# Kernel optimization log

Measured on AMD Instinct MI355X. Metric: run time of the kernel, lower is better.

## Reference

```python
import jax, jax.numpy as jnp
import numpy as np

NUM_HEADS = 16
EMBED_DIM = 1024
HEAD_DIM = EMBED_DIM // NUM_HEADS
DILATION = 4


def setup_inputs() -> dict:
    key = jax.random.key(0)
    ks = jax.random.split(key, 9)
    B, S, E = 2, 4096, EMBED_DIM
    scale = 1.0 / np.sqrt(E)
    inp = {
        "x": jax.random.normal(ks[0], (B, S, E), dtype=jnp.float32),
        "Wq": jax.random.normal(ks[1], (E, E), dtype=jnp.float32) * scale,
        "bq": jnp.zeros((E,), dtype=jnp.float32),
        "Wk": jax.random.normal(ks[2], (E, E), dtype=jnp.float32) * scale,
        "bk": jnp.zeros((E,), dtype=jnp.float32),
        "Wv": jax.random.normal(ks[3], (E, E), dtype=jnp.float32) * scale,
        "bv": jnp.zeros((E,), dtype=jnp.float32),
        "Wo": jax.random.normal(ks[4], (E, E), dtype=jnp.float32) * scale,
        "bo": jnp.zeros((E,), dtype=jnp.float32),
    }
    return inp


def reference(x, Wq, bq, Wk, bk, Wv, bv, Wo, bo):
    B, S, E = x.shape
    H, D = NUM_HEADS, HEAD_DIM

    def split_heads(t):  # [B,S,E] -> [B,H,S,D]
        return t.reshape(B, S, H, D).transpose(0, 2, 1, 3)

    q = split_heads(x @ Wq + bq)
    k = split_heads(x @ Wk + bk)[:, :, ::DILATION, :]   # dilated keys
    v = split_heads(x @ Wv + bv)[:, :, ::DILATION, :]   # dilated values

    scores = jnp.einsum('bhqd,bhkd->bhqk', q, k) / np.sqrt(D).astype(x.dtype)
    attn = jax.nn.softmax(scores, axis=-1)
    ctx = jnp.einsum('bhqk,bhkd->bhqd', attn, v)
    ctx = ctx.transpose(0, 2, 1, 3).reshape(B, S, E)
    return ctx @ Wo + bo
```

## Files before the change

kernel.cpp:

```cpp
#include <hip/hip_runtime.h>
#include <cstdint>
#include <cstddef>

typedef unsigned short u16;
typedef __attribute__((ext_vector_type(4))) float f32x4;
typedef __attribute__((ext_vector_type(8))) short short8;
typedef __attribute__((ext_vector_type(4))) unsigned short u16x4;
typedef short8 __attribute__((may_alias)) short8_a;
typedef uint2 __attribute__((may_alias)) uint2_a;

#define NH 16
#define ED 1024
#define HD 64
#define SEQ 4096
#define SKV 1024

#define QSCALE 0.1803368801111204f

__device__ __forceinline__ u16 f2bf(float f) {
  unsigned u = __builtin_bit_cast(unsigned, f);
  u += 0x7fffu + ((u >> 16) & 1u);
  return (u16)(u >> 16);
}

__device__ __forceinline__ float fexp2(float x) {
  float r;
  asm("v_exp_f32 %0, %1" : "=v"(r) : "v"(x));
  return r;
}

__device__ __forceinline__ unsigned cvtpk(float lo, float hi) {
  unsigned r;
  asm("v_cvt_pk_bf16_f32 %0, %1, %2" : "=v"(r) : "v"(lo), "v"(hi));
  return r;
}

__device__ __forceinline__ void gload16(const void* g, void* l) {
  __builtin_amdgcn_global_load_lds((const __attribute__((address_space(1))) void*)g,
                                   (__attribute__((address_space(3))) void*)l, 16, 0, 0);
}

__device__ __forceinline__ f32x4 mfma16(short8 a, short8 b, f32x4 c) {
  return __builtin_amdgcn_mfma_f32_16x16x32_bf16(a, b, c, 0, 0, 0);
}

__global__ __launch_bounds__(256) void prep_kernel(
    const float* __restrict__ x, u16* __restrict__ x16,
    const float* __restrict__ Wq, const float* __restrict__ Wk,
    const float* __restrict__ Wv, const float* __restrict__ Wo,
    u16* __restrict__ Wqt, u16* __restrict__ Wkt,
    u16* __restrict__ Wvt, u16* __restrict__ Wot) {
  __shared__ float t[64][65];
  int bx = blockIdx.x;
  if (bx < 8192) {
    int i = bx * 256 + threadIdx.x;
    f32x4 v = ((const f32x4*)x)[i];
    u16x4 o;
#pragma unroll
    for (int j = 0; j < 4; ++j) o[j] = f2bf(v[j]);
    ((u16x4*)x16)[i] = o;
    return;
  }
  int tt = bx - 8192;
  int wi = tt >> 8;
  tt &= 255;
  const float* W = (wi == 0) ? Wq : (wi == 1) ? Wk : (wi == 2) ? Wv : Wo;
  u16* Wt = (wi == 0) ? Wqt : (wi == 1) ? Wkt : (wi == 2) ? Wvt : Wot;
  int kb = (tt >> 4) * 64, nb = (tt & 15) * 64;
  int tx = threadIdx.x & 15, ty = threadIdx.x >> 4;
#pragma unroll
  for (int j = 0; j < 4; ++j) {
    int row = ty + j * 16;
    f32x4 v = *(const f32x4*)&W[(size_t)(kb + row) * ED + nb + tx * 4];
#pragma unroll
    for (int i = 0; i < 4; ++i) t[row][tx * 4 + i] = v[i];
  }
  __syncthreads();
#pragma unroll
  for (int j = 0; j < 4; ++j) {
    int n = ty + j * 16;
    u16x4 o;
#pragma unroll
    for (int i = 0; i < 4; ++i) o[i] = f2bf(t[tx * 4 + i][n]);
    *(u16x4*)&Wt[(size_t)(nb + n) * ED + kb + tx * 4] = o;
  }
}

__global__ __launch_bounds__(256) void qkv_gemm(
    const u16* __restrict__ A,
    const u16* __restrict__ Wqt, const u16* __restrict__ Wkt, const u16* __restrict__ Wvt,
    const float* __restrict__ bq, const float* __restrict__ bk, const float* __restrict__ bv,
    u16* __restrict__ Q16, u16* __restrict__ K16, u16* __restrict__ VT16) {
  __shared__ u16 Al[128 * 32];
  __shared__ u16 Bl[128 * 32];
  const int tid = threadIdx.x;
  const int w = tid >> 6, lane = tid & 63;
  const int by = blockIdx.y;
  int which, mblk;
  if (by < 64) { which = 0; mblk = by; }
  else if (by < 80) { which = 1; mblk = by - 64; }
  else { which = 2; mblk = by - 80; }
  const int rowmult = (which == 0) ? 1 : 4;
  const u16* Bt = (which == 0) ? Wqt : (which == 1) ? Wkt : Wvt;
  const float* bias = (which == 0) ? bq : (which == 1) ? bk : bv;
  const int m0 = mblk * 128, n0 = blockIdx.x * 128;
  const int wr = w >> 1, wc = w & 1;
  f32x4 acc[4][4];
#pragma unroll
  for (int i = 0; i < 4; ++i)
#pragma unroll
    for (int j = 0; j < 4; ++j) acc[i][j] = (f32x4){0.f, 0.f, 0.f, 0.f};

  const int srow = w * 16 + (lane >> 2);
  const int scol = (lane & 3) * 8;
  const u16* Ag0 = A + (size_t)(m0 + srow) * rowmult * ED + scol;
  const u16* Ag1 = A + (size_t)(m0 + srow + 64) * rowmult * ED + scol;
  const u16* Bg0 = Bt + (size_t)(n0 + srow) * ED + scol;
  const u16* Bg1 = Bt + (size_t)(n0 + srow + 64) * ED + scol;
  u16* Al0 = &Al[(w * 16) * 32];
  u16* Al1 = &Al[(64 + w * 16) * 32];
  u16* Bl0 = &Bl[(w * 16) * 32];
  u16* Bl1 = &Bl[(64 + w * 16) * 32];

  for (int k0 = 0; k0 < ED; k0 += 32) {
    gload16(Ag0 + k0, Al0);
    gload16(Ag1 + k0, Al1);
    gload16(Bg0 + k0, Bl0);
    gload16(Bg1 + k0, Bl1);
    __syncthreads();
    short8 af[4], bfr[4];
#pragma unroll
    for (int i = 0; i < 4; ++i)
      af[i] = *(const short8*)&Al[(wr * 64 + i * 16 + (lane & 15)) * 32 + (lane >> 4) * 8];
#pragma unroll
    for (int i = 0; i < 4; ++i)
      bfr[i] = *(const short8*)&Bl[(wc * 64 + i * 16 + (lane & 15)) * 32 + (lane >> 4) * 8];
#pragma unroll
    for (int i = 0; i < 4; ++i)
#pragma unroll
      for (int j = 0; j < 4; ++j)
        acc[i][j] = mfma16(af[i], bfr[j], acc[i][j]);
    __syncthreads();
  }

  const int r0 = m0 + wr * 64, c0g = n0 + wc * 64;
  if (which == 0 || which == 1) {
    u16* o = (which == 0) ? Q16 : K16;
    const int sxlog2 = (which == 0) ? 12 : 10;
    const int Sx = 1 << sxlog2;
    const float scl = (which == 0) ? QSCALE : 1.0f;
#pragma unroll
    for (int i = 0; i < 4; ++i) {
#pragma unroll
      for (int j = 0; j < 4; ++j) {
        int Cc = c0g + j * 16 + (lane & 15);
        int h = Cc >> 6, d = Cc & 63;
        float bv2 = bias[Cc];
#pragma unroll
        for (int r = 0; r < 4; ++r) {
          int R = r0 + i * 16 + (lane >> 4) * 4 + r;
          int b = R >> sxlog2, s = R & (Sx - 1);
          o[(((size_t)b * NH + h) * Sx + s) * HD + d] = f2bf((acc[i][j][r] + bv2) * scl);
        }
      }
    }
  } else {
    u16* o = VT16;
#pragma unroll
    for (int i = 0; i < 4; ++i) {
#pragma unroll
      for (int j = 0; j < 4; ++j) {
        int Cc = c0g + j * 16 + (lane & 15);
        int h = Cc >> 6, d = Cc & 63;
        float bv2 = bias[Cc];
#pragma unroll
        for (int r = 0; r < 4; ++r) {
          int R = r0 + i * 16 + (lane >> 4) * 4 + r;
          int b = R >> 10, s = R & 1023;
          o[(((size_t)b * NH + h) * HD + d) * SKV + s] = f2bf(acc[i][j][r] + bv2);
        }
      }
    }
  }
}

__global__ __launch_bounds__(256) void out_gemm(const u16* __restrict__ A,
                                                const u16* __restrict__ Bt,
                                                const float* __restrict__ bias,
                                                float* __restrict__ o) {
  __shared__ u16 Al[128 * 32];
  __shared__ u16 Bl[128 * 32];
  const int tid = threadIdx.x;
  const int w = tid >> 6, lane = tid & 63;
  const int m0 = blockIdx.y * 128, n0 = blockIdx.x * 128;
  const int wr = w >> 1, wc = w & 1;
  f32x4 acc[4][4];
#pragma unroll
  for (int i = 0; i < 4; ++i)
#pragma unroll
    for (int j = 0; j < 4; ++j) acc[i][j] = (f32x4){0.f, 0.f, 0.f, 0.f};

  const int srow = w * 16 + (lane >> 2);
  const int scol = (lane & 3) * 8;
  const u16* Ag0 = A + (size_t)(m0 + srow) * ED + scol;
  const u16* Ag1 = A + (size_t)(m0 + srow + 64) * ED + scol;
  const u16* Bg0 = Bt + (size_t)(n0 + srow) * ED + scol;
  const u16* Bg1 = Bt + (size_t)(n0 + srow + 64) * ED + scol;
  u16* Al0 = &Al[(w * 16) * 32];
  u16* Al1 = &Al[(64 + w * 16) * 32];
  u16* Bl0 = &Bl[(w * 16) * 32];
  u16* Bl1 = &Bl[(64 + w * 16) * 32];

  for (int k0 = 0; k0 < ED; k0 += 32) {
    gload16(Ag0 + k0, Al0);
    gload16(Ag1 + k0, Al1);
    gload16(Bg0 + k0, Bl0);
    gload16(Bg1 + k0, Bl1);
    __syncthreads();
    short8 af[4], bfr[4];
#pragma unroll
    for (int i = 0; i < 4; ++i)
      af[i] = *(const short8*)&Al[(wr * 64 + i * 16 + (lane & 15)) * 32 + (lane >> 4) * 8];
#pragma unroll
    for (int i = 0; i < 4; ++i)
      bfr[i] = *(const short8*)&Bl[(wc * 64 + i * 16 + (lane & 15)) * 32 + (lane >> 4) * 8];
#pragma unroll
    for (int i = 0; i < 4; ++i)
#pragma unroll
      for (int j = 0; j < 4; ++j)
        acc[i][j] = mfma16(af[i], bfr[j], acc[i][j]);
    __syncthreads();
  }

  const int r0 = m0 + wr * 64, c0g = n0 + wc * 64;
#pragma unroll
  for (int i = 0; i < 4; ++i) {
#pragma unroll
    for (int j = 0; j < 4; ++j) {
      int Cc = c0g + j * 16 + (lane & 15);
      float bv2 = bias[Cc];
#pragma unroll
      for (int r = 0; r < 4; ++r) {
        int R = r0 + i * 16 + (lane >> 4) * 4 + r;
        o[(size_t)R * ED + Cc] = acc[i][j][r] + bv2;
      }
    }
  }
}

__global__ __launch_bounds__(256) void attn_kernel(const u16* __restrict__ Q,
                                                   const u16* __restrict__ K,
                                                   const u16* __restrict__ VT,
                                                   u16* __restrict__ ctx) {
  __shared__ u16 Kl[2][64 * 64];
  __shared__ u16 Vl[2][64 * 64];
  __shared__ u16 Pl[4 * 16 * 64];
  const int tid = threadIdx.x, w = tid >> 6, lane = tid & 63;
  const int qt = blockIdx.x, bh = blockIdx.y, b = bh >> 4, h = bh & 15;

  const u16* Qp = Q + ((size_t)bh * SEQ + qt * 64 + w * 16) * HD;
  short8 qf0 = *(const short8_a*)&Qp[(lane & 15) * HD + (lane >> 4) * 8];
  short8 qf1 = *(const short8_a*)&Qp[(lane & 15) * HD + (lane >> 4) * 8 + 32];
  const u16* Kb = K + (size_t)bh * SKV * HD;
  const u16* VTb = VT + (size_t)bh * HD * SKV;

  float lp = 0.f;
  f32x4 cacc[4];
#pragma unroll
  for (int i = 0; i < 4; ++i) cacc[i] = (f32x4){0.f, 0.f, 0.f, 0.f};

  const int srow = lane >> 3;
  const int scolswz = ((lane & 7) ^ (lane >> 3)) * 8;
  const int g4 = lane >> 4;
  const int sw7 = lane & 7;
  const int q = lane & 15;

  int poff[4];
#pragma unroll
  for (int fk = 0; fk < 4; ++fk) {
    int gr = 2 * fk + (g4 >> 1);
    poff[fk] = q * 64 + ((gr ^ sw7) * 8) + 4 * (g4 & 1);
  }

  auto stage = [&](int buf, int kt) {
    gload16(Kb + ((size_t)kt * 64 + w * 8 + srow) * HD + scolswz, &Kl[buf][(w * 8) * 64]);
    gload16(Kb + ((size_t)kt * 64 + 32 + w * 8 + srow) * HD + scolswz, &Kl[buf][(32 + w * 8) * 64]);
    gload16(VTb + (size_t)(w * 8 + srow) * SKV + kt * 64 + scolswz, &Vl[buf][(w * 8) * 64]);
    gload16(VTb + (size_t)(32 + w * 8 + srow) * SKV + kt * 64 + scolswz, &Vl[buf][(32 + w * 8) * 64]);
  };

  stage(0, 0);
  u16* Pw = &Pl[w * 1024];

  for (int kt = 0; kt < 16; ++kt) {
    const int cur = kt & 1;
    __syncthreads();
    if (kt < 15) stage(cur ^ 1, kt + 1);
    const u16* Kc = Kl[cur];
    const u16* Vc = Vl[cur];

    f32x4 sv[4];
    __builtin_amdgcn_s_setprio(1);
#pragma unroll
    for (int fk = 0; fk < 4; ++fk) {
      const int kr = fk * 16 + (lane & 15);
      short8 a0 = *(const short8_a*)&Kc[kr * 64 + ((g4 ^ sw7) * 8)];
      short8 a1 = *(const short8_a*)&Kc[kr * 64 + (((g4 + 4) ^ sw7) * 8)];
      f32x4 z = (f32x4){0.f, 0.f, 0.f, 0.f};
      z = mfma16(a0, qf0, z);
      z = mfma16(a1, qf1, z);
      sv[fk] = z;
    }
    __builtin_amdgcn_s_setprio(0);

#pragma unroll
    for (int fk = 0; fk < 4; ++fk) {
      float p0 = fexp2(sv[fk][0]);
      float p1 = fexp2(sv[fk][1]);
      float p2 = fexp2(sv[fk][2]);
      float p3 = fexp2(sv[fk][3]);
      lp += (p0 + p1) + (p2 + p3);
      uint2 pk;
      pk.x = cvtpk(p0, p1);
      pk.y = cvtpk(p2, p3);
      *(uint2_a*)&Pw[poff[fk]] = pk;
    }

    short8 pa0 = *(const short8_a*)&Pw[(lane & 15) * 64 + ((g4 ^ sw7) * 8)];
    short8 pa1 = *(const short8_a*)&Pw[(lane & 15) * 64 + (((g4 + 4) ^ sw7) * 8)];
    __builtin_amdgcn_s_setprio(1);
#pragma unroll
    for (int fd = 0; fd < 4; ++fd) {
      const int vrow = fd * 16 + (lane & 15);
      short8 vb0 = *(const short8_a*)&Vc[vrow * 64 + ((g4 ^ sw7) * 8)];
      short8 vb1 = *(const short8_a*)&Vc[vrow * 64 + (((g4 + 4) ^ sw7) * 8)];
      cacc[fd] = mfma16(pa0, vb0, cacc[fd]);
      cacc[fd] = mfma16(pa1, vb1, cacc[fd]);
    }
    __builtin_amdgcn_s_setprio(0);
  }

  lp += __shfl_xor(lp, 16);
  lp += __shfl_xor(lp, 32);

  const int q0 = qt * 64 + w * 16 + (lane >> 4) * 4;
#pragma unroll
  for (int r = 0; r < 4; ++r) {
    float inv = 1.f / __shfl(lp, (lane >> 4) * 4 + r);
#pragma unroll
    for (int fd = 0; fd < 4; ++fd) {
      int d = fd * 16 + (lane & 15);
      ctx[((size_t)b * SEQ + q0 + r) * ED + h * HD + d] = f2bf(cacc[fd][r] * inv);
    }
  }
}

extern "C" void kernel_launch(void* const* d_in, const int* in_sizes, int n_in,
                              void* d_out, int out_size, void* d_ws, size_t ws_size,
                              hipStream_t stream) {
  (void)in_sizes; (void)n_in; (void)out_size; (void)ws_size;
  const float* x  = (const float*)d_in[0];
  const float* Wq = (const float*)d_in[1];
  const float* bq = (const float*)d_in[2];
  const float* Wk = (const float*)d_in[3];
  const float* bk = (const float*)d_in[4];
  const float* Wv = (const float*)d_in[5];
  const float* bv = (const float*)d_in[6];
  const float* Wo = (const float*)d_in[7];
  const float* bo = (const float*)d_in[8];

  char* ws = (char*)d_ws;
  u16* x16 = (u16*)(ws);
  u16* Wqt = (u16*)(ws + (16ull << 20));
  u16* Wkt = (u16*)(ws + (18ull << 20));
  u16* Wvt = (u16*)(ws + (20ull << 20));
  u16* Wot = (u16*)(ws + (22ull << 20));
  u16* Q16 = (u16*)(ws + (24ull << 20));
  u16* K16 = (u16*)(ws + (40ull << 20));
  u16* VT16 = (u16*)(ws + (44ull << 20));
  u16* ctx16 = x16;

  prep_kernel<<<9216, 256, 0, stream>>>(x, x16, Wq, Wk, Wv, Wo, Wqt, Wkt, Wvt, Wot);

  qkv_gemm<<<dim3(8, 96), 256, 0, stream>>>(x16, Wqt, Wkt, Wvt, bq, bk, bv,
                                            Q16, K16, VT16);

  attn_kernel<<<dim3(64, 32), 256, 0, stream>>>(Q16, K16, VT16, ctx16);

  out_gemm<<<dim3(8, 64), 256, 0, stream>>>(ctx16, Wot, bo, (float*)d_out);
}
```

Before: 237.2 us.

## Remap blocks for XCD locality and read K/V fragments directly from global

All three main kernels now remap the flat block index so that consecutive logical tiles land on the same XCD, which is meant to improve L2 reuse of shared operands (weights, or the K/V of one head). The attention kernel also drops the LDS double-buffered staging of K and V and the per-tile __syncthreads. Each wave instead loads its MFMA fragments straight from global memory and relies on cache hits from neighbouring blocks on the same XCD. The trade is less LDS use and no barriers against more global and L2 traffic per wave, with latency that is no longer hidden by prefetch.

```diff
diff --git a/kernel.cpp b/kernel.cpp
--- a/kernel.cpp
+++ b/kernel.cpp
@@ -95,7 +95,9 @@
   __shared__ u16 Bl[128 * 32];
   const int tid = threadIdx.x;
   const int w = tid >> 6, lane = tid & 63;
-  const int by = blockIdx.y;
+  int flat = blockIdx.x + 8 * blockIdx.y;
+  int nf = (flat & 7) * 96 + (flat >> 3);
+  const int bxs = nf & 7, by = nf >> 3;
   int which, mblk;
   if (by < 64) { which = 0; mblk = by; }
   else if (by < 80) { which = 1; mblk = by - 64; }
@@ -103,7 +105,7 @@
   const int rowmult = (which == 0) ? 1 : 4;
   const u16* Bt = (which == 0) ? Wqt : (which == 1) ? Wkt : Wvt;
   const float* bias = (which == 0) ? bq : (which == 1) ? bk : bv;
-  const int m0 = mblk * 128, n0 = blockIdx.x * 128;
+  const int m0 = mblk * 128, n0 = bxs * 128;
   const int wr = w >> 1, wc = w & 1;
   f32x4 acc[4][4];
 #pragma unroll
@@ -192,7 +194,9 @@
   __shared__ u16 Bl[128 * 32];
   const int tid = threadIdx.x;
   const int w = tid >> 6, lane = tid & 63;
-  const int m0 = blockIdx.y * 128, n0 = blockIdx.x * 128;
+  int flat = blockIdx.x + 8 * blockIdx.y;
+  int nf = (flat & 7) * 64 + (flat >> 3);
+  const int m0 = (nf >> 3) * 128, n0 = (nf & 7) * 128;
   const int wr = w >> 1, wc = w & 1;
   f32x4 acc[4][4];
 #pragma unroll
@@ -252,29 +256,28 @@
                                                    const u16* __restrict__ K,
                                                    const u16* __restrict__ VT,
                                                    u16* __restrict__ ctx) {
-  __shared__ u16 Kl[2][64 * 64];
-  __shared__ u16 Vl[2][64 * 64];
   __shared__ u16 Pl[4 * 16 * 64];
   const int tid = threadIdx.x, w = tid >> 6, lane = tid & 63;
-  const int qt = blockIdx.x, bh = blockIdx.y, b = bh >> 4, h = bh & 15;
+  int flat = blockIdx.x;
+  int nf = (flat & 7) * 256 + (flat >> 3);
+  const int bh = nf >> 6, qt = nf & 63;
+  const int b = bh >> 4, h = bh & 15;
 
   const u16* Qp = Q + ((size_t)bh * SEQ + qt * 64 + w * 16) * HD;
-  short8 qf0 = *(const short8_a*)&Qp[(lane & 15) * HD + (lane >> 4) * 8];
-  short8 qf1 = *(const short8_a*)&Qp[(lane & 15) * HD + (lane >> 4) * 8 + 32];
-  const u16* Kb = K + (size_t)bh * SKV * HD;
-  const u16* VTb = VT + (size_t)bh * HD * SKV;
-
-  float lp = 0.f;
-  f32x4 cacc[4];
-#pragma unroll
-  for (int i = 0; i < 4; ++i) cacc[i] = (f32x4){0.f, 0.f, 0.f, 0.f};
-
-  const int srow = lane >> 3;
-  const int scolswz = ((lane & 7) ^ (lane >> 3)) * 8;
   const int g4 = lane >> 4;
   const int sw7 = lane & 7;
   const int q = lane & 15;
 
+  short8 qf0 = *(const short8_a*)&Qp[(lane & 15) * HD + g4 * 8];
+  short8 qf1 = *(const short8_a*)&Qp[(lane & 15) * HD + g4 * 8 + 32];
+  const u16* Kb = K + (size_t)bh * SKV * HD;
+  const u16* VTb = VT + (size_t)bh * HD * SKV;
+
+  float lp = 0.f;
+  f32x4 cacc[4];
+#pragma unroll
+  for (int i = 0; i < 4; ++i) cacc[i] = (f32x4){0.f, 0.f, 0.f, 0.f};
+
   int poff[4];
 #pragma unroll
   for (int fk = 0; fk < 4; ++fk) {
@@ -282,30 +285,18 @@
     poff[fk] = q * 64 + ((gr ^ sw7) * 8) + 4 * (g4 & 1);
   }
 
-  auto stage = [&](int buf, int kt) {
-    gload16(Kb + ((size_t)kt * 64 + w * 8 + srow) * HD + scolswz, &Kl[buf][(w * 8) * 64]);
-    gload16(Kb + ((size_t)kt * 64 + 32 + w * 8 + srow) * HD + scolswz, &Kl[buf][(32 + w * 8) * 64]);
-    gload16(VTb + (size_t)(w * 8 + srow) * SKV + kt * 64 + scolswz, &Vl[buf][(w * 8) * 64]);
-    gload16(VTb + (size_t)(32 + w * 8 + srow) * SKV + kt * 64 + scolswz, &Vl[buf][(32 + w * 8) * 64]);
-  };
-
-  stage(0, 0);
   u16* Pw = &Pl[w * 1024];
+  const u16* Kfrag = Kb + (size_t)(lane & 15) * HD + g4 * 8;
+  const u16* Vfrag = VTb + (size_t)(lane & 15) * SKV + g4 * 8;
 
   for (int kt = 0; kt < 16; ++kt) {
-    const int cur = kt & 1;
-    __syncthreads();
-    if (kt < 15) stage(cur ^ 1, kt + 1);
-    const u16* Kc = Kl[cur];
-    const u16* Vc = Vl[cur];
-
     f32x4 sv[4];
     __builtin_amdgcn_s_setprio(1);
 #pragma unroll
     for (int fk = 0; fk < 4; ++fk) {
-      const int kr = fk * 16 + (lane & 15);
-      short8 a0 = *(const short8_a*)&Kc[kr * 64 + ((g4 ^ sw7) * 8)];
-      short8 a1 = *(const short8_a*)&Kc[kr * 64 + (((g4 + 4) ^ sw7) * 8)];
+      const u16* kr = Kfrag + (size_t)(kt * 64 + fk * 16) * HD;
+      short8 a0 = *(const short8_a*)kr;
+      short8 a1 = *(const short8_a*)(kr + 32);
       f32x4 z = (f32x4){0.f, 0.f, 0.f, 0.f};
       z = mfma16(a0, qf0, z);
       z = mfma16(a1, qf1, z);
@@ -331,9 +322,9 @@
     __builtin_amdgcn_s_setprio(1);
 #pragma unroll
     for (int fd = 0; fd < 4; ++fd) {
-      const int vrow = fd * 16 + (lane & 15);
-      short8 vb0 = *(const short8_a*)&Vc[vrow * 64 + ((g4 ^ sw7) * 8)];
-      short8 vb1 = *(const short8_a*)&Vc[vrow * 64 + (((g4 + 4) ^ sw7) * 8)];
+      const u16* vr = Vfrag + (size_t)(fd * 16) * SKV + kt * 64;
+      short8 vb0 = *(const short8_a*)vr;
+      short8 vb1 = *(const short8_a*)(vr + 32);
       cacc[fd] = mfma16(pa0, vb0, cacc[fd]);
       cacc[fd] = mfma16(pa1, vb1, cacc[fd]);
     }
@@ -385,7 +376,7 @@
   qkv_gemm<<<dim3(8, 96), 256, 0, stream>>>(x16, Wqt, Wkt, Wvt, bq, bk, bv,
                                             Q16, K16, VT16);
 
-  attn_kernel<<<dim3(64, 32), 256, 0, stream>>>(Q16, K16, VT16, ctx16);
+  attn_kernel<<<2048, 256, 0, stream>>>(Q16, K16, VT16, ctx16);
 
   out_gemm<<<dim3(8, 64), 256, 0, stream>>>(ctx16, Wot, bo, (float*)d_out);
 }
```

Measured after the change: 400.3 us. +68.8%, slower.

## Double query rows per attention wave and remap block order for XCD locality

Applied to the files above, without the earlier changes.

The attention kernel now has each wave handle 32 query rows instead of 16, so every K/V tile staged into shared memory serves twice as many queries. The grid shrinks to 1024 blocks. The QKV and output GEMMs, and attention, also remap the flat block index so that consecutive hardware-dispatched blocks (round-robin across 8 XCDs) share operand tiles and get better L2 locality. The cost is more registers per wave for accumulators and fewer blocks to fill the device.

```diff
diff --git a/kernel.cpp b/kernel.cpp
--- a/kernel.cpp
+++ b/kernel.cpp
@@ -95,7 +95,9 @@
   __shared__ u16 Bl[128 * 32];
   const int tid = threadIdx.x;
   const int w = tid >> 6, lane = tid & 63;
-  const int by = blockIdx.y;
+  int flat = blockIdx.x + 8 * blockIdx.y;
+  int nf = (flat & 7) * 96 + (flat >> 3);
+  const int bxs = nf & 7, by = nf >> 3;
   int which, mblk;
   if (by < 64) { which = 0; mblk = by; }
   else if (by < 80) { which = 1; mblk = by - 64; }
@@ -103,7 +105,7 @@
   const int rowmult = (which == 0) ? 1 : 4;
   const u16* Bt = (which == 0) ? Wqt : (which == 1) ? Wkt : Wvt;
   const float* bias = (which == 0) ? bq : (which == 1) ? bk : bv;
-  const int m0 = mblk * 128, n0 = blockIdx.x * 128;
+  const int m0 = mblk * 128, n0 = bxs * 128;
   const int wr = w >> 1, wc = w & 1;
   f32x4 acc[4][4];
 #pragma unroll
@@ -192,7 +194,9 @@
   __shared__ u16 Bl[128 * 32];
   const int tid = threadIdx.x;
   const int w = tid >> 6, lane = tid & 63;
-  const int m0 = blockIdx.y * 128, n0 = blockIdx.x * 128;
+  int flat = blockIdx.x + 8 * blockIdx.y;
+  int nf = (flat & 7) * 64 + (flat >> 3);
+  const int m0 = (nf >> 3) * 128, n0 = (nf & 7) * 128;
   const int wr = w >> 1, wc = w & 1;
   f32x4 acc[4][4];
 #pragma unroll
@@ -256,25 +260,35 @@
   __shared__ u16 Vl[2][64 * 64];
   __shared__ u16 Pl[4 * 16 * 64];
   const int tid = threadIdx.x, w = tid >> 6, lane = tid & 63;
-  const int qt = blockIdx.x, bh = blockIdx.y, b = bh >> 4, h = bh & 15;
-
-  const u16* Qp = Q + ((size_t)bh * SEQ + qt * 64 + w * 16) * HD;
-  short8 qf0 = *(const short8_a*)&Qp[(lane & 15) * HD + (lane >> 4) * 8];
-  short8 qf1 = *(const short8_a*)&Qp[(lane & 15) * HD + (lane >> 4) * 8 + 32];
-  const u16* Kb = K + (size_t)bh * SKV * HD;
-  const u16* VTb = VT + (size_t)bh * HD * SKV;
-
-  float lp = 0.f;
-  f32x4 cacc[4];
-#pragma unroll
-  for (int i = 0; i < 4; ++i) cacc[i] = (f32x4){0.f, 0.f, 0.f, 0.f};
-
-  const int srow = lane >> 3;
-  const int scolswz = ((lane & 7) ^ (lane >> 3)) * 8;
+  int flat = blockIdx.x;
+  int nf = (flat & 7) * 128 + (flat >> 3);
+  const int bh = nf >> 5, qt = nf & 31;
+  const int b = bh >> 4, h = bh & 15;
+
   const int g4 = lane >> 4;
   const int sw7 = lane & 7;
   const int q = lane & 15;
 
+  const u16* Qp = Q + ((size_t)bh * SEQ + qt * 128 + w * 32) * HD;
+  short8 qf[2][2];
+#pragma unroll
+  for (int u = 0; u < 2; ++u) {
+    qf[u][0] = *(const short8_a*)&Qp[(u * 16 + q) * HD + g4 * 8];
+    qf[u][1] = *(const short8_a*)&Qp[(u * 16 + q) * HD + g4 * 8 + 32];
+  }
+  const u16* Kb = K + (size_t)bh * SKV * HD;
+  const u16* VTb = VT + (size_t)bh * HD * SKV;
+
+  float lp[2] = {0.f, 0.f};
+  f32x4 cacc[2][4];
+#pragma unroll
+  for (int u = 0; u < 2; ++u)
+#pragma unroll
+    for (int i = 0; i < 4; ++i) cacc[u][i] = (f32x4){0.f, 0.f, 0.f, 0.f};
+
+  const int srow = lane >> 3;
+  const int scolswz = ((lane & 7) ^ (lane >> 3)) * 8;
+
   int poff[4];
 #pragma unroll
   for (int fk = 0; fk < 4; ++fk) {
@@ -282,75 +296,89 @@
     poff[fk] = q * 64 + ((gr ^ sw7) * 8) + 4 * (g4 & 1);
   }
 
-  auto stage = [&](int buf, int kt) {
-    gload16(Kb + ((size_t)kt * 64 + w * 8 + srow) * HD + scolswz, &Kl[buf][(w * 8) * 64]);
-    gload16(Kb + ((size_t)kt * 64 + 32 + w * 8 + srow) * HD + scolswz, &Kl[buf][(32 + w * 8) * 64]);
-    gload16(VTb + (size_t)(w * 8 + srow) * SKV + kt * 64 + scolswz, &Vl[buf][(w * 8) * 64]);
-    gload16(VTb + (size_t)(32 + w * 8 + srow) * SKV + kt * 64 + scolswz, &Vl[buf][(32 + w * 8) * 64]);
+  const u16* gK0 = Kb + (size_t)(w * 8 + srow) * HD + scolswz;
+  const u16* gK1 = Kb + (size_t)(32 + w * 8 + srow) * HD + scolswz;
+  const u16* gV0 = VTb + (size_t)(w * 8 + srow) * SKV + scolswz;
+  const u16* gV1 = VTb + (size_t)(32 + w * 8 + srow) * SKV + scolswz;
+
+  auto stage = [&](int buf) {
+    gload16(gK0, &Kl[buf][(w * 8) * 64]);
+    gload16(gK1, &Kl[buf][(32 + w * 8) * 64]);
+    gload16(gV0, &Vl[buf][(w * 8) * 64]);
+    gload16(gV1, &Vl[buf][(32 + w * 8) * 64]);
+    gK0 += 64 * HD; gK1 += 64 * HD; gV0 += 64; gV1 += 64;
   };
 
-  stage(0, 0);
+  stage(0);
   u16* Pw = &Pl[w * 1024];
 
   for (int kt = 0; kt < 16; ++kt) {
     const int cur = kt & 1;
     __syncthreads();
-    if (kt < 15) stage(cur ^ 1, kt + 1);
+    if (kt < 15) stage(cur ^ 1);
     const u16* Kc = Kl[cur];
     const u16* Vc = Vl[cur];
 
-    f32x4 sv[4];
+    f32x4 sv[2][4];
     __builtin_amdgcn_s_setprio(1);
 #pragma unroll
     for (int fk = 0; fk < 4; ++fk) {
-      const int kr = fk * 16 + (lane & 15);
+      const int kr = fk * 16 + q;
       short8 a0 = *(const short8_a*)&Kc[kr * 64 + ((g4 ^ sw7) * 8)];
       short8 a1 = *(const short8_a*)&Kc[kr * 64 + (((g4 + 4) ^ sw7) * 8)];
-      f32x4 z = (f32x4){0.f, 0.f, 0.f, 0.f};
-      z = mfma16(a0, qf0, z);
-      z = mfma16(a1, qf1, z);
-      sv[fk] = z;
+#pragma unroll
+      for (int u = 0; u < 2; ++u) {
+        f32x4 z = (f32x4){0.f, 0.f, 0.f, 0.f};
+        z = mfma16(a0, qf[u][0], z);
+        z = mfma16(a1, qf[u][1], z);
+        sv[u][fk] = z;
+      }
     }
     __builtin_amdgcn_s_setprio(0);
 
 #pragma unroll
-    for (int fk = 0; fk < 4; ++fk) {
-      float p0 = fexp2(sv[fk][0]);
-      float p1 = fexp2(sv[fk][1]);
-      float p2 = fexp2(sv[fk][2]);
-      float p3 = fexp2(sv[fk][3]);
-      lp += (p0 + p1) + (p2 + p3);
-      uint2 pk;
-      pk.x = cvtpk(p0, p1);
-      pk.y = cvtpk(p2, p3);
-      *(uint2_a*)&Pw[poff[fk]] = pk;
-    }
-
-    short8 pa0 = *(const short8_a*)&Pw[(lane & 15) * 64 + ((g4 ^ sw7) * 8)];
-    short8 pa1 = *(const short8_a*)&Pw[(lane & 15) * 64 + (((g4 + 4) ^ sw7) * 8)];
-    __builtin_amdgcn_s_setprio(1);
-#pragma unroll
-    for (int fd = 0; fd < 4; ++fd) {
-      const int vrow = fd * 16 + (lane & 15);
-      short8 vb0 = *(const short8_a*)&Vc[vrow * 64 + ((g4 ^ sw7) * 8)];
-      short8 vb1 = *(const short8_a*)&Vc[vrow * 64 + (((g4 + 4) ^ sw7) * 8)];
-      cacc[fd] = mfma16(pa0, vb0, cacc[fd]);
-      cacc[fd] = mfma16(pa1, vb1, cacc[fd]);
-    }
-    __builtin_amdgcn_s_setprio(0);
-  }
-
-  lp += __shfl_xor(lp, 16);
-  lp += __shfl_xor(lp, 32);
-
-  const int q0 = qt * 64 + w * 16 + (lane >> 4) * 4;
-#pragma unroll
-  for (int r = 0; r < 4; ++r) {
-    float inv = 1.f / __shfl(lp, (lane >> 4) * 4 + r);
-#pragma unroll
-    for (int fd = 0; fd < 4; ++fd) {
-      int d = fd * 16 + (lane & 15);
-      ctx[((size_t)b * SEQ + q0 + r) * ED + h * HD + d] = f2bf(cacc[fd][r] * inv);
+    for (int u = 0; u < 2; ++u) {
+#pragma unroll
+      for (int fk = 0; fk < 4; ++fk) {
+        float p0 = fexp2(sv[u][fk][0]);
+        float p1 = fexp2(sv[u][fk][1]);
+        float p2 = fexp2(sv[u][fk][2]);
+        float p3 = fexp2(sv[u][fk][3]);
+        lp[u] += (p0 + p1) + (p2 + p3);
+        uint2 pk;
+        pk.x = cvtpk(p0, p1);
+        pk.y = cvtpk(p2, p3);
+        *(uint2_a*)&Pw[poff[fk]] = pk;
+      }
+      short8 pa0 = *(const short8_a*)&Pw[q * 64 + ((g4 ^ sw7) * 8)];
+      short8 pa1 = *(const short8_a*)&Pw[q * 64 + (((g4 + 4) ^ sw7) * 8)];
+      __builtin_amdgcn_s_setprio(1);
+#pragma unroll
+      for (int fd = 0; fd < 4; ++fd) {
+        const int vrow = fd * 16 + q;
+        short8 vb0 = *(const short8_a*)&Vc[vrow * 64 + ((g4 ^ sw7) * 8)];
+        short8 vb1 = *(const short8_a*)&Vc[vrow * 64 + (((g4 + 4) ^ sw7) * 8)];
+        cacc[u][fd] = mfma16(pa0, vb0, cacc[u][fd]);
+        cacc[u][fd] = mfma16(pa1, vb1, cacc[u][fd]);
+      }
+      __builtin_amdgcn_s_setprio(0);
+    }
+  }
+
+#pragma unroll
+  for (int u = 0; u < 2; ++u) {
+    float l = lp[u];
+    l += __shfl_xor(l, 16);
+    l += __shfl_xor(l, 32);
+    const int q0 = qt * 128 + w * 32 + u * 16 + (lane >> 4) * 4;
+#pragma unroll
+    for (int r = 0; r < 4; ++r) {
+      float inv = 1.f / __shfl(l, (lane >> 4) * 4 + r);
+#pragma unroll
+      for (int fd = 0; fd < 4; ++fd) {
+        int d = fd * 16 + q;
+        ctx[((size_t)b * SEQ + q0 + r) * ED + h * HD + d] = f2bf(cacc[u][fd][r] * inv);
+      }
     }
   }
 }
@@ -385,7 +413,7 @@
   qkv_gemm<<<dim3(8, 96), 256, 0, stream>>>(x16, Wqt, Wkt, Wvt, bq, bk, bv,
                                             Q16, K16, VT16);
 
-  attn_kernel<<<dim3(64, 32), 256, 0, stream>>>(Q16, K16, VT16, ctx16);
+  attn_kernel<<<1024, 256, 0, stream>>>(Q16, K16, VT16, ctx16);
 
   out_gemm<<<dim3(8, 64), 256, 0, stream>>>(ctx16, Wot, bo, (float*)d_out);
 }
```

Result: faster. 229.3 us (-3.3%).
